# Performance work log

Measured on AMD Instinct MI355X. Metric: run time of the kernel, lower is better.

The kernel has to match this reference:

```python
import jax, jax.numpy as jnp
import numpy as np

BS, N, D_IN, HID, D_OUT = 16, 256, 128, 128, 128


def setup_inputs() -> dict:
    key = jax.random.key(0)
    ks = jax.random.split(key, 10)
    s = 0.02
    return {
        "x": jax.random.normal(ks[0], (BS, N, D_IN), dtype=jnp.float32),
        "adj": jax.random.randint(ks[1], (BS, N, N), 0, 2, dtype=jnp.int32),
        "W_fc": jax.random.normal(ks[2], (D_IN, HID), dtype=jnp.float32) * s,
        "b_fc": jnp.zeros((HID,), dtype=jnp.float32),
        "W_a1": jax.random.normal(ks[3], (2 * HID, HID), dtype=jnp.float32) * s,
        "b_a1": jnp.zeros((HID,), dtype=jnp.float32),
        "w_a2": jax.random.normal(ks[4], (HID,), dtype=jnp.float32) * s,
        "b_a2": jnp.zeros((), dtype=jnp.float32),
        "W_out": jax.random.normal(ks[5], (HID, D_OUT), dtype=jnp.float32) * s,
        "b_out": jnp.zeros((D_OUT,), dtype=jnp.float32),
    }


def reference(x, adj, W_fc, b_fc, W_a1, b_a1, w_a2, b_a2, W_out, b_out):
    # h = fc(x): (bs, n, hid)
    h = jnp.einsum("bnd,dh->bnh", x, W_fc) + b_fc
    # attn first layer on concat([h_i, h_j]) decomposes into two half-projections
    # (same math as Linear(2*hid, hid) on the concatenated pair features).
    a_i = jnp.einsum("bnh,hk->bnk", h, W_a1[:HID])  # contribution of h_i
    a_j = jnp.einsum("bnh,hk->bnk", h, W_a1[HID:])  # contribution of h_j
    pre = a_i[:, :, None, :] + a_j[:, None, :, :] + b_a1  # (bs, n, n, hid)
    e = jnp.einsum("bijk,k->bij", jax.nn.relu(pre), w_a2) + b_a2  # (bs, n, n)
    e = jnp.where(adj == 0, jnp.float32(-1e9), e)
    attn = jax.nn.softmax(e, axis=-1)
    h_prime = jnp.einsum("bij,bjh->bih", attn, h)
    out = jnp.einsum("bih,ho->bio", h_prime, W_out) + b_out
    return out
```

## Files before the change

kernel.cpp:

```cpp
#include <hip/hip_runtime.h>

#define BS  16
#define NN  256
#define HID 128

__device__ __forceinline__ int xcd_swz(int bid) {
    return (bid & 7) * 128 + (bid >> 3);
}

__global__ __launch_bounds__(256, 4) void gat_k1(
    const float* __restrict__ x, const float* __restrict__ W_fc,
    const float* __restrict__ b_fc, const float* __restrict__ W_a1,
    const float* __restrict__ b_a1, const float* __restrict__ W_out,
    float* __restrict__ ai, float* __restrict__ ajT, float* __restrict__ g)
{
    __shared__ __align__(16) float xs[4 * HID];
    __shared__ __align__(16) float hs[4 * HID];
    __shared__ __align__(16) float ajtmp[4 * HID];

    const int tid = threadIdx.x;
    const int k   = tid & 127;
    const int q   = tid >> 7;
    const int swz = xcd_swz(blockIdx.x);
    const int r0  = swz * 4;
    const int b   = r0 >> 8;
    const int n0  = r0 & 255;

    if (tid < 128)
        *(float4*)&xs[tid * 4] = *(const float4*)&x[r0 * HID + tid * 4];
    __syncthreads();

    {
        const float bf = b_fc[k];
        float a0a = bf, a0b = 0.f, a1a = bf, a1b = 0.f;
        #pragma unroll 4
        for (int d0 = 0; d0 < HID; d0 += 8) {
            float w[8];
            #pragma unroll
            for (int t = 0; t < 8; ++t) w[t] = W_fc[(d0 + t) * HID + k];
            const float4 xA0 = *(const float4*)&xs[(2 * q + 0) * HID + d0];
            const float4 xA1 = *(const float4*)&xs[(2 * q + 0) * HID + d0 + 4];
            const float4 xB0 = *(const float4*)&xs[(2 * q + 1) * HID + d0];
            const float4 xB1 = *(const float4*)&xs[(2 * q + 1) * HID + d0 + 4];
            a0a += xA0.x * w[0] + xA0.y * w[1] + xA0.z * w[2] + xA0.w * w[3];
            a0b += xA1.x * w[4] + xA1.y * w[5] + xA1.z * w[6] + xA1.w * w[7];
            a1a += xB0.x * w[0] + xB0.y * w[1] + xB0.z * w[2] + xB0.w * w[3];
            a1b += xB1.x * w[4] + xB1.y * w[5] + xB1.z * w[6] + xB1.w * w[7];
        }
        hs[(2 * q + 0) * HID + k] = a0a + a0b;
        hs[(2 * q + 1) * HID + k] = a1a + a1b;
    }
    __syncthreads();

    {
        const float* Wp  = W_a1 + q * HID * HID;
        const float bias = q ? 0.f : b_a1[k];
        float acc[4][2];
        #pragma unroll
        for (int r = 0; r < 4; ++r) { acc[r][0] = bias; acc[r][1] = 0.f; }
        #pragma unroll 2
        for (int d0 = 0; d0 < HID; d0 += 8) {
            float w[8];
            #pragma unroll
            for (int t = 0; t < 8; ++t) w[t] = Wp[(d0 + t) * HID + k];
            #pragma unroll
            for (int r = 0; r < 4; ++r) {
                const float4 h0 = *(const float4*)&hs[r * HID + d0];
                const float4 h1 = *(const float4*)&hs[r * HID + d0 + 4];
                acc[r][0] += h0.x * w[0] + h0.y * w[1] + h0.z * w[2] + h0.w * w[3];
                acc[r][1] += h1.x * w[4] + h1.y * w[5] + h1.z * w[6] + h1.w * w[7];
            }
        }
        if (!q) {
            #pragma unroll
            for (int r = 0; r < 4; ++r)
                ai[(r0 + r) * HID + k] = acc[r][0] + acc[r][1];
        } else {
            #pragma unroll
            for (int r = 0; r < 4; ++r)
                ajtmp[r * HID + k] = acc[r][0] + acc[r][1];
        }
    }

    {
        float a0a = 0.f, a0b = 0.f, a1a = 0.f, a1b = 0.f;
        #pragma unroll 4
        for (int d0 = 0; d0 < HID; d0 += 8) {
            float w[8];
            #pragma unroll
            for (int t = 0; t < 8; ++t) w[t] = W_out[(d0 + t) * HID + k];
            const float4 hA0 = *(const float4*)&hs[(2 * q + 0) * HID + d0];
            const float4 hA1 = *(const float4*)&hs[(2 * q + 0) * HID + d0 + 4];
            const float4 hB0 = *(const float4*)&hs[(2 * q + 1) * HID + d0];
            const float4 hB1 = *(const float4*)&hs[(2 * q + 1) * HID + d0 + 4];
            a0a += hA0.x * w[0] + hA0.y * w[1] + hA0.z * w[2] + hA0.w * w[3];
            a0b += hA1.x * w[4] + hA1.y * w[5] + hA1.z * w[6] + hA1.w * w[7];
            a1a += hB0.x * w[0] + hB0.y * w[1] + hB0.z * w[2] + hB0.w * w[3];
            a1b += hB1.x * w[4] + hB1.y * w[5] + hB1.z * w[6] + hB1.w * w[7];
        }
        g[(r0 + 2 * q + 0) * HID + k] = a0a + a0b;
        g[(r0 + 2 * q + 1) * HID + k] = a1a + a1b;
    }
    __syncthreads();

    {
        const int kk = tid >> 1;
        const int jj = (tid & 1) * 2;
        float2 v;
        v.x = ajtmp[(jj + 0) * HID + kk];
        v.y = ajtmp[(jj + 1) * HID + kk];
        *(float2*)&ajT[(b * HID + kk) * NN + n0 + jj] = v;
    }
}

__global__ __launch_bounds__(256, 4) void gat_k2(
    const float* __restrict__ ai, const float* __restrict__ ajT,
    const float* __restrict__ g,  const int* __restrict__ adj,
    const float* __restrict__ w_a2, const float* __restrict__ b_a2,
    const float* __restrict__ b_out, float* __restrict__ out)
{
    __shared__ __align__(16) float4 aw4[HID];
    __shared__ __align__(16) float  w2s[HID];
    __shared__ __align__(16) float  ep[4][NN];
    __shared__ __align__(16) float  red[2][4][HID];

    const int tid = threadIdx.x;
    const int swz = xcd_swz(blockIdx.x);
    const int b   = swz >> 6;
    const int i0  = (swz & 63) * 4;
    const int wv  = tid >> 6, lane = tid & 63;

    if (tid < 128) {
        float4 v;
        v.x = ai[(b * NN + i0 + 0) * HID + tid];
        v.y = ai[(b * NN + i0 + 1) * HID + tid];
        v.z = ai[(b * NN + i0 + 2) * HID + tid];
        v.w = ai[(b * NN + i0 + 3) * HID + tid];
        aw4[tid] = v;
        w2s[tid] = w_a2[tid];
    }
    __syncthreads();

    const int j = wv * 64 + lane;
    {
        const float* ajp = ajT + b * HID * NN + j;
        float acc[4] = {0.f, 0.f, 0.f, 0.f};
        #pragma unroll 8
        for (int kk = 0; kk < HID; ++kk) {
            const float a  = ajp[kk * NN];
            const float4 av = aw4[kk];
            const float wk = w2s[kk];
            acc[0] += fmaxf(av.x + a, 0.f) * wk;
            acc[1] += fmaxf(av.y + a, 0.f) * wk;
            acc[2] += fmaxf(av.z + a, 0.f) * wk;
            acc[3] += fmaxf(av.w + a, 0.f) * wk;
        }
        const float ba2 = b_a2[0];
        #pragma unroll
        for (int r = 0; r < 4; ++r) {
            const int am = adj[(b * NN + i0 + r) * NN + j];
            ep[r][j] = am ? acc[r] + ba2 : -1e9f;
        }
    }
    __syncthreads();

    {
        float4 e4 = *(const float4*)&ep[wv][4 * lane];
        float m = fmaxf(fmaxf(e4.x, e4.y), fmaxf(e4.z, e4.w));
        #pragma unroll
        for (int off = 32; off; off >>= 1) m = fmaxf(m, __shfl_xor(m, off));
        const float p0 = __expf(e4.x - m), p1 = __expf(e4.y - m);
        const float p2 = __expf(e4.z - m), p3 = __expf(e4.w - m);
        float s = (p0 + p1) + (p2 + p3);
        #pragma unroll
        for (int off = 32; off; off >>= 1) s += __shfl_xor(s, off);
        const float inv = 1.f / s;
        const float4 pv = {p0 * inv, p1 * inv, p2 * inv, p3 * inv};
        *(float4*)&ep[wv][4 * lane] = pv;
    }
    __syncthreads();

    const int k = tid & 127, qh = tid >> 7;
    {
        float o[4] = {0.f, 0.f, 0.f, 0.f};
        const float* gb = g + (b * NN + qh * 128) * HID + k;
        const int jb = qh * 128;
        #pragma unroll 2
        for (int jq = 0; jq < 128; jq += 4) {
            const float g0 = gb[(jq + 0) * HID];
            const float g1 = gb[(jq + 1) * HID];
            const float g2 = gb[(jq + 2) * HID];
            const float g3 = gb[(jq + 3) * HID];
            const float4 pA = *(const float4*)&ep[0][jb + jq];
            const float4 pB = *(const float4*)&ep[1][jb + jq];
            const float4 pC = *(const float4*)&ep[2][jb + jq];
            const float4 pD = *(const float4*)&ep[3][jb + jq];
            o[0] += pA.x * g0 + pA.y * g1 + pA.z * g2 + pA.w * g3;
            o[1] += pB.x * g0 + pB.y * g1 + pB.z * g2 + pB.w * g3;
            o[2] += pC.x * g0 + pC.y * g1 + pC.z * g2 + pC.w * g3;
            o[3] += pD.x * g0 + pD.y * g1 + pD.z * g2 + pD.w * g3;
        }
        #pragma unroll
        for (int r = 0; r < 4; ++r) red[qh][r][k] = o[r];
    }
    __syncthreads();

    {
        const float bo = b_out[k];
        #pragma unroll
        for (int r2 = 0; r2 < 2; ++r2) {
            const int r = 2 * qh + r2;
            out[(b * NN + i0 + r) * HID + k] =
                red[0][r][k] + red[1][r][k] + bo;
        }
    }
}

extern "C" void kernel_launch(void* const* d_in, const int* in_sizes, int n_in,
                              void* d_out, int out_size, void* d_ws, size_t ws_size,
                              hipStream_t stream) {
    const float* x     = (const float*)d_in[0];
    const int*   adj   = (const int*)  d_in[1];
    const float* W_fc  = (const float*)d_in[2];
    const float* b_fc  = (const float*)d_in[3];
    const float* W_a1  = (const float*)d_in[4];
    const float* b_a1  = (const float*)d_in[5];
    const float* w_a2  = (const float*)d_in[6];
    const float* b_a2  = (const float*)d_in[7];
    const float* W_out = (const float*)d_in[8];
    const float* b_out = (const float*)d_in[9];
    float* out = (float*)d_out;

    float* ws  = (float*)d_ws;
    float* ai  = ws;
    float* ajT = ws + BS * NN * HID;
    float* g   = ws + 2 * BS * NN * HID;

    gat_k1<<<BS * NN / 4, 256, 0, stream>>>(x, W_fc, b_fc, W_a1, b_a1, W_out,
                                            ai, ajT, g);
    gat_k2<<<BS * (NN / 4), 256, 0, stream>>>(ai, ajT, g, adj, w_a2, b_a2,
                                              b_out, out);
}
```

Measured before the change: 42.88 us.

## Store ai transposed and read wave-uniform operands via scalar loads instead of LDS

```diff
diff --git a/kernel.cpp b/kernel.cpp
--- a/kernel.cpp
+++ b/kernel.cpp
@@ -12,11 +12,9 @@
     const float* __restrict__ x, const float* __restrict__ W_fc,
     const float* __restrict__ b_fc, const float* __restrict__ W_a1,
     const float* __restrict__ b_a1, const float* __restrict__ W_out,
-    float* __restrict__ ai, float* __restrict__ ajT, float* __restrict__ g)
+    float* __restrict__ aiT, float* __restrict__ ajT, float* __restrict__ g)
 {
-    __shared__ __align__(16) float xs[4 * HID];
     __shared__ __align__(16) float hs[4 * HID];
-    __shared__ __align__(16) float ajtmp[4 * HID];
 
     const int tid = threadIdx.x;
     const int k   = tid & 127;
@@ -26,9 +24,8 @@
     const int b   = r0 >> 8;
     const int n0  = r0 & 255;
 
-    if (tid < 128)
-        *(float4*)&xs[tid * 4] = *(const float4*)&x[r0 * HID + tid * 4];
-    __syncthreads();
+    const float* x0 = x + __builtin_amdgcn_readfirstlane((r0 + 2 * q) * HID);
+    const float* x1 = x0 + HID;
 
     {
         const float bf = b_fc[k];
@@ -38,14 +35,10 @@
             float w[8];
             #pragma unroll
             for (int t = 0; t < 8; ++t) w[t] = W_fc[(d0 + t) * HID + k];
-            const float4 xA0 = *(const float4*)&xs[(2 * q + 0) * HID + d0];
-            const float4 xA1 = *(const float4*)&xs[(2 * q + 0) * HID + d0 + 4];
-            const float4 xB0 = *(const float4*)&xs[(2 * q + 1) * HID + d0];
-            const float4 xB1 = *(const float4*)&xs[(2 * q + 1) * HID + d0 + 4];
-            a0a += xA0.x * w[0] + xA0.y * w[1] + xA0.z * w[2] + xA0.w * w[3];
-            a0b += xA1.x * w[4] + xA1.y * w[5] + xA1.z * w[6] + xA1.w * w[7];
-            a1a += xB0.x * w[0] + xB0.y * w[1] + xB0.z * w[2] + xB0.w * w[3];
-            a1b += xB1.x * w[4] + xB1.y * w[5] + xB1.z * w[6] + xB1.w * w[7];
+            a0a += x0[d0+0]*w[0] + x0[d0+1]*w[1] + x0[d0+2]*w[2] + x0[d0+3]*w[3];
+            a0b += x0[d0+4]*w[4] + x0[d0+5]*w[5] + x0[d0+6]*w[6] + x0[d0+7]*w[7];
+            a1a += x1[d0+0]*w[0] + x1[d0+1]*w[1] + x1[d0+2]*w[2] + x1[d0+3]*w[3];
+            a1b += x1[d0+4]*w[4] + x1[d0+5]*w[5] + x1[d0+6]*w[6] + x1[d0+7]*w[7];
         }
         hs[(2 * q + 0) * HID + k] = a0a + a0b;
         hs[(2 * q + 1) * HID + k] = a1a + a1b;
@@ -71,15 +64,10 @@
                 acc[r][1] += h1.x * w[4] + h1.y * w[5] + h1.z * w[6] + h1.w * w[7];
             }
         }
-        if (!q) {
-            #pragma unroll
-            for (int r = 0; r < 4; ++r)
-                ai[(r0 + r) * HID + k] = acc[r][0] + acc[r][1];
-        } else {
-            #pragma unroll
-            for (int r = 0; r < 4; ++r)
-                ajtmp[r * HID + k] = acc[r][0] + acc[r][1];
-        }
+        float* dst = (q ? ajT : aiT) + (b * HID + k) * NN + n0;
+        const float4 v = {acc[0][0] + acc[0][1], acc[1][0] + acc[1][1],
+                          acc[2][0] + acc[2][1], acc[3][0] + acc[3][1]};
+        *(float4*)dst = v;
     }
 
     {
@@ -101,66 +89,46 @@
         g[(r0 + 2 * q + 0) * HID + k] = a0a + a0b;
         g[(r0 + 2 * q + 1) * HID + k] = a1a + a1b;
     }
-    __syncthreads();
-
-    {
-        const int kk = tid >> 1;
-        const int jj = (tid & 1) * 2;
-        float2 v;
-        v.x = ajtmp[(jj + 0) * HID + kk];
-        v.y = ajtmp[(jj + 1) * HID + kk];
-        *(float2*)&ajT[(b * HID + kk) * NN + n0 + jj] = v;
-    }
 }
 
 __global__ __launch_bounds__(256, 4) void gat_k2(
-    const float* __restrict__ ai, const float* __restrict__ ajT,
+    const float* __restrict__ aiT, const float* __restrict__ ajT,
     const float* __restrict__ g,  const int* __restrict__ adj,
     const float* __restrict__ w_a2, const float* __restrict__ b_a2,
     const float* __restrict__ b_out, float* __restrict__ out)
 {
-    __shared__ __align__(16) float4 aw4[HID];
-    __shared__ __align__(16) float  w2s[HID];
-    __shared__ __align__(16) float  ep[4][NN];
-    __shared__ __align__(16) float  red[2][4][HID];
+    __shared__ __align__(16) float ep[4][NN];
+    __shared__ __align__(16) float red[2][4][HID];
 
     const int tid = threadIdx.x;
     const int swz = xcd_swz(blockIdx.x);
     const int b   = swz >> 6;
     const int i0  = (swz & 63) * 4;
     const int wv  = tid >> 6, lane = tid & 63;
-
-    if (tid < 128) {
-        float4 v;
-        v.x = ai[(b * NN + i0 + 0) * HID + tid];
-        v.y = ai[(b * NN + i0 + 1) * HID + tid];
-        v.z = ai[(b * NN + i0 + 2) * HID + tid];
-        v.w = ai[(b * NN + i0 + 3) * HID + tid];
-        aw4[tid] = v;
-        w2s[tid] = w_a2[tid];
-    }
-    __syncthreads();
-
-    const int j = wv * 64 + lane;
+    const int j   = wv * 64 + lane;
+
+    int am[4];
+    #pragma unroll
+    for (int r = 0; r < 4; ++r) am[r] = adj[(b * NN + i0 + r) * NN + j];
+
     {
         const float* ajp = ajT + b * HID * NN + j;
+        const float* aip = aiT + __builtin_amdgcn_readfirstlane(b * HID * NN + i0);
         float acc[4] = {0.f, 0.f, 0.f, 0.f};
         #pragma unroll 8
         for (int kk = 0; kk < HID; ++kk) {
-            const float a  = ajp[kk * NN];
-            const float4 av = aw4[kk];
-            const float wk = w2s[kk];
-            acc[0] += fmaxf(av.x + a, 0.f) * wk;
-            acc[1] += fmaxf(av.y + a, 0.f) * wk;
-            acc[2] += fmaxf(av.z + a, 0.f) * wk;
-            acc[3] += fmaxf(av.w + a, 0.f) * wk;
+            const float a   = ajp[kk * NN];
+            const float4 s4 = *(const float4*)&aip[kk * NN];
+            const float wk  = w_a2[kk];
+            acc[0] += fmaxf(s4.x + a, 0.f) * wk;
+            acc[1] += fmaxf(s4.y + a, 0.f) * wk;
+            acc[2] += fmaxf(s4.z + a, 0.f) * wk;
+            acc[3] += fmaxf(s4.w + a, 0.f) * wk;
         }
         const float ba2 = b_a2[0];
         #pragma unroll
-        for (int r = 0; r < 4; ++r) {
-            const int am = adj[(b * NN + i0 + r) * NN + j];
-            ep[r][j] = am ? acc[r] + ba2 : -1e9f;
-        }
+        for (int r = 0; r < 4; ++r)
+            ep[r][j] = am[r] ? acc[r] + ba2 : -1e9f;
     }
     __syncthreads();
 
@@ -185,7 +153,7 @@
         float o[4] = {0.f, 0.f, 0.f, 0.f};
         const float* gb = g + (b * NN + qh * 128) * HID + k;
         const int jb = qh * 128;
-        #pragma unroll 2
+        #pragma unroll 4
         for (int jq = 0; jq < 128; jq += 4) {
             const float g0 = gb[(jq + 0) * HID];
             const float g1 = gb[(jq + 1) * HID];
@@ -232,12 +200,12 @@
     float* out = (float*)d_out;
 
     float* ws  = (float*)d_ws;
-    float* ai  = ws;
+    float* aiT = ws;
     float* ajT = ws + BS * NN * HID;
     float* g   = ws + 2 * BS * NN * HID;
 
     gat_k1<<<BS * NN / 4, 256, 0, stream>>>(x, W_fc, b_fc, W_a1, b_a1, W_out,
-                                            ai, ajT, g);
-    gat_k2<<<BS * (NN / 4), 256, 0, stream>>>(ai, ajT, g, adj, w_a2, b_a2,
+                                            aiT, ajT, g);
+    gat_k2<<<BS * (NN / 4), 256, 0, stream>>>(aiT, ajT, g, adj, w_a2, b_a2,
                                               b_out, out);
 }
```

Result: slower. 43.88 us (+2.3%).
